# Kernel tuning notes

Hardware: AMD Instinct MI355X
Metric: run time of the kernel (lower is better)

## Reference

```python
import jax, jax.numpy as jnp
import numpy as np

NEG_SLOPE = 0.2
EPS = 1e-12


def _spmm(edge_row, edge_col, edge_w, h, n):
    # out[i] = sum_{e: row=i} w_e * h[col_e]   (row-normalized adjacency @ h)
    msgs = edge_w[:, None] * h[edge_col]
    return jax.ops.segment_sum(msgs, edge_row, num_segments=n)


def setup_inputs() -> dict:
    key = jax.random.key(0)
    ks = jax.random.split(key, 6)
    n, e, c_in, c_hid, c_out = 50000, 1600000, 300, 2048, 2048
    x = jax.random.normal(ks[0], (n, c_in), dtype=jnp.float32)
    # xavier-uniform-like init
    W1 = jax.random.uniform(ks[1], (c_in, c_hid), jnp.float32, -1.0, 1.0) * np.sqrt(6.0 / (c_in + c_hid))
    b1 = jnp.zeros((c_hid,), jnp.float32)
    W2 = jax.random.uniform(ks[2], (c_hid, c_out), jnp.float32, -1.0, 1.0) * np.sqrt(6.0 / (c_hid + c_out))
    b2 = jnp.zeros((c_out,), jnp.float32)
    edge_row = jax.random.randint(ks[3], (e,), 0, n, dtype=jnp.int32)
    edge_col = jax.random.randint(ks[4], (e,), 0, n, dtype=jnp.int32)
    return {"x": x, "W1": W1, "b1": b1, "W2": W2, "b2": b2,
            "edge_row": edge_row, "edge_col": edge_col}


def reference(x, W1, b1, W2, b2, edge_row, edge_col):
    n = x.shape[0]
    # 'in' normalization of unit-weight adjacency: w_e = 1 / in_degree(row_e)
    deg = jax.ops.segment_sum(jnp.ones_like(edge_row, dtype=jnp.float32), edge_row, num_segments=n)
    edge_w = 1.0 / jnp.maximum(deg, 1.0)
    edge_w = edge_w[edge_row]
    # layer 1: adj @ (x @ W1) + b1, LeakyReLU(0.2)  (dropout is identity in eval)
    h = _spmm(edge_row, edge_col, edge_w, x @ W1, n) + b1
    h = jnp.where(h >= 0, h, NEG_SLOPE * h)
    # last layer: no relu
    h = _spmm(edge_row, edge_col, edge_w, h @ W2, n) + b2
    # F.normalize: row-wise L2 with eps clamp
    norm = jnp.maximum(jnp.sqrt(jnp.sum(h * h, axis=-1, keepdims=True)), EPS)
    return h / norm
```

## Files before the change

### kernel.cpp

```cpp
#include <hip/hip_runtime.h>
#include <math.h>

typedef unsigned short ushort_t;
using bf16x8  = __attribute__((ext_vector_type(8))) short;
using f32x4   = __attribute__((ext_vector_type(4))) float;
using ushort8 = __attribute__((ext_vector_type(8))) unsigned short;

__device__ __forceinline__ unsigned short f2bf(float f) {
    union { float f; unsigned int u; } v; v.f = f;
    unsigned int r = v.u + 0x7FFFu + ((v.u >> 16) & 1u);
    return (unsigned short)(r >> 16);
}
__device__ __forceinline__ float bf2f(unsigned short u) {
    union { unsigned int u; float f; } v; v.u = ((unsigned int)u) << 16;
    return v.f;
}

#if defined(__has_builtin)
#if __has_builtin(__builtin_amdgcn_cvt_f32_fp8) && __has_builtin(__builtin_amdgcn_cvt_pk_fp8_f32)
#define FP8_HW 1
#endif
#endif

__device__ __forceinline__ unsigned char f2fp8(float v) {
#ifdef FP8_HW
    unsigned int p = __builtin_amdgcn_cvt_pk_fp8_f32(v, v, 0, false);
    return (unsigned char)(p & 0xFFu);
#else
    union { float f; unsigned u; } b; b.f = v;
    unsigned s = (b.u >> 24) & 0x80u;
    float a = fabsf(v);
    if (a >= 448.f) return (unsigned char)(s | 0x7E);
    if (a < 0.015625f) {
        int m = (int)rintf(a * 512.0f);
        if (m >= 8) return (unsigned char)(s | 0x08);
        return (unsigned char)(s | (unsigned)m);
    }
    unsigned u = b.u & 0x7FFFFFFFu;
    u += 0x7FFFFu + ((u >> 20) & 1u);
    int e8 = (int)((u >> 23) & 0xFF) - 120;
    unsigned M = (u >> 20) & 7u;
    if (e8 > 15 || (e8 == 15 && M == 7u)) return (unsigned char)(s | 0x7E);
    return (unsigned char)(s | ((unsigned)e8 << 3) | M);
#endif
}

#ifdef FP8_HW
#define ACC8(ac, w) do { \
    ac[0] += __builtin_amdgcn_cvt_f32_fp8((int)(w).x, 0); \
    ac[1] += __builtin_amdgcn_cvt_f32_fp8((int)(w).x, 1); \
    ac[2] += __builtin_amdgcn_cvt_f32_fp8((int)(w).x, 2); \
    ac[3] += __builtin_amdgcn_cvt_f32_fp8((int)(w).x, 3); \
    ac[4] += __builtin_amdgcn_cvt_f32_fp8((int)(w).y, 0); \
    ac[5] += __builtin_amdgcn_cvt_f32_fp8((int)(w).y, 1); \
    ac[6] += __builtin_amdgcn_cvt_f32_fp8((int)(w).y, 2); \
    ac[7] += __builtin_amdgcn_cvt_f32_fp8((int)(w).y, 3); \
} while (0)
#else
__device__ __forceinline__ float fp82f(unsigned u) {
    unsigned s = u >> 7, e = (u >> 3) & 15u, m = u & 7u;
    union { unsigned u; float f; } nb;
    nb.u = (s << 31) | ((e + 120u) << 23) | (m << 20);
    float sub = (float)(int)m * 0.001953125f;
    sub = s ? -sub : sub;
    return e ? nb.f : sub;
}
#define ACC8(ac, w) do { \
    ac[0] += fp82f(((w).x      ) & 0xFFu); \
    ac[1] += fp82f(((w).x >>  8) & 0xFFu); \
    ac[2] += fp82f(((w).x >> 16) & 0xFFu); \
    ac[3] += fp82f(((w).x >> 24)        ); \
    ac[4] += fp82f(((w).y      ) & 0xFFu); \
    ac[5] += fp82f(((w).y >>  8) & 0xFFu); \
    ac[6] += fp82f(((w).y >> 16) & 0xFFu); \
    ac[7] += fp82f(((w).y >> 24)        ); \
} while (0)
#endif

typedef const __attribute__((address_space(1))) void* gas_ptr;
typedef __attribute__((address_space(3))) void* las_ptr;
__device__ __forceinline__ void gload16(const void* g, void* l) {
    __builtin_amdgcn_global_load_lds((gas_ptr)g, (las_ptr)l, 16, 0, 0);
}


__global__ void k_zero_i32(int* __restrict__ p, int n) {
    int i = blockIdx.x * blockDim.x + threadIdx.x;
    if (i < n) p[i] = 0;
}

__global__ void k_count_deg(const int* __restrict__ erow, int* __restrict__ deg, int e) {
    for (int i = blockIdx.x * blockDim.x + threadIdx.x; i < e; i += gridDim.x * blockDim.x)
        atomicAdd(&deg[erow[i]], 1);
}

__global__ __launch_bounds__(1024) void k_scan(const int* __restrict__ deg, int* __restrict__ ptr,
                                               int* __restrict__ cursor, int n) {
    __shared__ int buf[1024];
    __shared__ int carry_s;
    int t = threadIdx.x;
    if (t == 0) { carry_s = 0; ptr[0] = 0; }
    __syncthreads();
    for (int base = 0; base < n; base += 1024) {
        int i = base + t;
        int v = (i < n) ? deg[i] : 0;
        buf[t] = v;
        __syncthreads();
        #pragma unroll
        for (int off = 1; off < 1024; off <<= 1) {
            int xv = (t >= off) ? buf[t - off] : 0;
            __syncthreads();
            buf[t] += xv;
            __syncthreads();
        }
        int carry = carry_s;
        int incl = buf[t] + carry;
        if (i < n) { ptr[i + 1] = incl; cursor[i] = incl - v; }
        int bsum = buf[1023];
        __syncthreads();
        if (t == 0) carry_s = carry + bsum;
        __syncthreads();
    }
}

__global__ void k_scatter(const int* __restrict__ erow, const int* __restrict__ ecol,
                          int* __restrict__ cursor, int* __restrict__ csr_col, int e) {
    for (int i = blockIdx.x * blockDim.x + threadIdx.x; i < e; i += gridDim.x * blockDim.x) {
        int pos = atomicAdd(&cursor[erow[i]], 1);
        csr_col[pos] = ecol[i];
    }
}


__global__ __launch_bounds__(256) void k_cvt_wT(const float* __restrict__ W, unsigned short* __restrict__ WT,
                                                int K, int N, int Kpad) {
    __shared__ float tile[32][33];
    int kp0 = blockIdx.x * 32, n0 = blockIdx.y * 32;
    int tx = threadIdx.x & 31, ty = threadIdx.x >> 5;
    #pragma unroll
    for (int ii = 0; ii < 4; ++ii) {
        int k = kp0 + ty + ii * 8;
        tile[ty + ii * 8][tx] = (k < K) ? W[(size_t)k * N + n0 + tx] : 0.0f;
    }
    __syncthreads();
    #pragma unroll
    for (int ii = 0; ii < 4; ++ii) {
        int n = n0 + ty + ii * 8;
        WT[(size_t)n * Kpad + kp0 + tx] = f2bf(tile[tx][ty + ii * 8]);
    }
}


__global__ __launch_bounds__(128) void k_spmm1(const int* __restrict__ ptr, const int* __restrict__ col,
                                               const float* __restrict__ x, unsigned short* __restrict__ ax) {
    int r = blockIdx.x;
    int t = threadIdx.x;
    int s = ptr[r], e = ptr[r + 1];
    bool act = t < 75;
    const float4* xb = (const float4*)x;
    float4 a0 = {0.f, 0.f, 0.f, 0.f}, a1 = {0.f, 0.f, 0.f, 0.f};
    int p = s;
    for (; p + 1 < e; p += 2) {
        int c0 = col[p], c1 = col[p + 1];
        if (act) {
            float4 v0 = xb[(size_t)c0 * 75 + t];
            float4 v1 = xb[(size_t)c1 * 75 + t];
            a0.x += v0.x; a0.y += v0.y; a0.z += v0.z; a0.w += v0.w;
            a1.x += v1.x; a1.y += v1.y; a1.z += v1.z; a1.w += v1.w;
        }
    }
    if (p < e && act) {
        float4 v = xb[(size_t)col[p] * 75 + t];
        a0.x += v.x; a0.y += v.y; a0.z += v.z; a0.w += v.w;
    }
    float w = 1.0f / fmaxf((float)(e - s), 1.0f);
    unsigned short* o = ax + (size_t)r * 320;
    if (act) {
        ushort4 ov;
        ov.x = f2bf((a0.x + a1.x) * w);
        ov.y = f2bf((a0.y + a1.y) * w);
        ov.z = f2bf((a0.z + a1.z) * w);
        ov.w = f2bf((a0.w + a1.w) * w);
        *(ushort4*)(o + t * 4) = ov;
    } else if (t < 80) {
        ushort4 z = {0, 0, 0, 0};
        *(ushort4*)(o + t * 4) = z;
    }
}


template <int EPI>
__global__ __launch_bounds__(256) void k_mfma_gemm(const unsigned short* __restrict__ A, int lda,
                                                   const unsigned short* __restrict__ BT, int ldb,
                                                   const float* __restrict__ bias,
                                                   void* __restrict__ Cv,
                                                   int M, int N, int K) {
    __shared__ __align__(16) unsigned short As[128 * 32];
    __shared__ __align__(16) unsigned short Bs[128 * 32];
    int tid = threadIdx.x;
    int lane = tid & 63;
    int wid = tid >> 6;
    int wm = wid >> 1, wn = wid & 1;
    int bm = blockIdx.y * 128, bn = blockIdx.x * 128;

    f32x4 zero4 = {0.f, 0.f, 0.f, 0.f};
    f32x4 acc[4][4];
    #pragma unroll
    for (int i = 0; i < 4; ++i)
        #pragma unroll
        for (int j = 0; j < 4; ++j) acc[i][j] = zero4;

    int srow = tid >> 2;
    int scol = (tid & 3) * 8;
    int ar0 = bm + srow;      if (ar0 >= M) ar0 = M - 1;
    int ar1 = bm + srow + 64; if (ar1 >= M) ar1 = M - 1;
    const unsigned short* gA0 = A + (size_t)ar0 * lda + scol;
    const unsigned short* gA1 = A + (size_t)ar1 * lda + scol;
    const unsigned short* gB0 = BT + (size_t)(bn + srow) * ldb + scol;
    const unsigned short* gB1 = BT + (size_t)(bn + srow + 64) * ldb + scol;

    int kq = (lane >> 4) * 8;
    int rsel = lane & 15;

    for (int k0 = 0; k0 < K; k0 += 32) {
        gload16(gA0 + k0, &As[(size_t)tid * 8]);
        gload16(gA1 + k0, &As[(size_t)(tid + 256) * 8]);
        gload16(gB0 + k0, &Bs[(size_t)tid * 8]);
        gload16(gB1 + k0, &Bs[(size_t)(tid + 256) * 8]);
        __syncthreads();

        bf16x8 af[4], bfr[4];
        #pragma unroll
        for (int i = 0; i < 4; ++i) {
            af[i]  = *(const bf16x8*)&As[(wm * 64 + i * 16 + rsel) * 32 + kq];
            bfr[i] = *(const bf16x8*)&Bs[(wn * 64 + i * 16 + rsel) * 32 + kq];
        }
        #pragma unroll
        for (int i = 0; i < 4; ++i)
            #pragma unroll
            for (int j = 0; j < 4; ++j)
                acc[i][j] = __builtin_amdgcn_mfma_f32_16x16x32_bf16(af[i], bfr[j], acc[i][j], 0, 0, 0);
        __syncthreads();
    }

    #pragma unroll
    for (int i = 0; i < 4; ++i) {
        int row_base = bm + wm * 64 + i * 16 + (lane >> 4) * 4;
        #pragma unroll
        for (int j = 0; j < 4; ++j) {
            int colg = bn + wn * 64 + j * 16 + (lane & 15);
            float bv = (EPI == 1) ? bias[colg] : 0.0f;
            #pragma unroll
            for (int r = 0; r < 4; ++r) {
                int row = row_base + r;
                if (row < M) {
                    float v = acc[i][j][r];
                    if (EPI == 1) {
                        v += bv; v = (v >= 0.f) ? v : 0.2f * v;
                        ((unsigned short*)Cv)[(size_t)row * N + colg] = f2bf(v);
                    } else {
                        ((unsigned char*)Cv)[(size_t)row * N + colg] = f2fp8(v * 32.0f);
                    }
                }
            }
        }
    }
}


__global__ __launch_bounds__(256) void k_spmm2_norm(const int* __restrict__ ptr, const int* __restrict__ col,
                                                    const unsigned char* __restrict__ H2,
                                                    const float* __restrict__ b2,
                                                    float* __restrict__ out) {
    const int C = 2048;
    int r = blockIdx.x, t = threadIdx.x;
    int s = ptr[r], e = ptr[r + 1];
    float ac0[8] = {}, ac1[8] = {}, ac2[8] = {}, ac3[8] = {};
    const uint2* base = (const uint2*)(H2 + t * 8);
    int p = s;
    for (; p + 3 < e; p += 4) {
        uint2 w0 = base[(size_t)col[p]     * 256];
        uint2 w1 = base[(size_t)col[p + 1] * 256];
        uint2 w2 = base[(size_t)col[p + 2] * 256];
        uint2 w3 = base[(size_t)col[p + 3] * 256];
        ACC8(ac0, w0); ACC8(ac1, w1); ACC8(ac2, w2); ACC8(ac3, w3);
    }
    for (; p < e; ++p) {
        uint2 w = base[(size_t)col[p] * 256];
        ACC8(ac0, w);
    }
    float w = 1.0f / (32.0f * fmaxf((float)(e - s), 1.0f));
    float ss = 0.f;
    float vv[8];
    #pragma unroll
    for (int j = 0; j < 8; ++j) {
        float v = (ac0[j] + ac1[j] + ac2[j] + ac3[j]) * w + b2[t * 8 + j];
        vv[j] = v;
        ss += v * v;
    }
    __shared__ float red[4];
    __shared__ float scale_s;
    #pragma unroll
    for (int off = 32; off > 0; off >>= 1) ss += __shfl_down(ss, off, 64);
    int lane = t & 63, wid = t >> 6;
    if (lane == 0) red[wid] = ss;
    __syncthreads();
    if (t == 0) {
        float tot = red[0] + red[1] + red[2] + red[3];
        scale_s = 1.0f / fmaxf(sqrtf(tot), 1e-12f);
    }
    __syncthreads();
    float sc = scale_s;
    float* o = out + (size_t)r * C + t * 8;
    float4 o0 = {vv[0] * sc, vv[1] * sc, vv[2] * sc, vv[3] * sc};
    float4 o1 = {vv[4] * sc, vv[5] * sc, vv[6] * sc, vv[7] * sc};
    *(float4*)o = o0;
    *(float4*)(o + 4) = o1;
}


extern "C" void kernel_launch(void* const* d_in, const int* in_sizes, int n_in,
                              void* d_out, int out_size, void* d_ws, size_t ws_size,
                              hipStream_t stream) {
    const float* x  = (const float*)d_in[0];
    const float* W1 = (const float*)d_in[1];
    const float* b1 = (const float*)d_in[2];
    const float* W2 = (const float*)d_in[3];
    const float* b2 = (const float*)d_in[4];
    const int* erow = (const int*)d_in[5];
    const int* ecol = (const int*)d_in[6];

    const int chid = in_sizes[2];
    const int cout = in_sizes[4];
    const int cin  = in_sizes[1] / chid;
    const int n    = in_sizes[0] / cin;
    const int e    = in_sizes[5];
    const int cinp = (cin + 31) & ~31;

    char* ws = (char*)d_ws;
    size_t off = 0;
    auto alloc = [&](size_t bytes) -> void* {
        void* p = ws + off;
        off += (bytes + 255) & ~(size_t)255;
        return p;
    };
    int*            deg     = (int*)alloc((size_t)n * 4);
    int*            ptr     = (int*)alloc((size_t)(n + 1) * 4);
    int*            cursor  = (int*)alloc((size_t)n * 4);
    int*            csr_col = (int*)alloc((size_t)e * 4);
    unsigned short* ax      = (unsigned short*)alloc((size_t)n * cinp * 2);
    unsigned short* W1T     = (unsigned short*)alloc((size_t)chid * cinp * 2);
    unsigned short* W2T     = (unsigned short*)alloc((size_t)cout * chid * 2);
    unsigned char*  H2f8    = (unsigned char*)alloc((size_t)n * cout);
    unsigned short* H1      = (unsigned short*)d_out;

    k_zero_i32<<<(n + 255) / 256, 256, 0, stream>>>(deg, n);
    k_count_deg<<<2048, 256, 0, stream>>>(erow, deg, e);
    k_scan<<<1, 1024, 0, stream>>>(deg, ptr, cursor, n);
    k_scatter<<<2048, 256, 0, stream>>>(erow, ecol, cursor, csr_col, e);

    dim3 gw1(cinp / 32, chid / 32);
    k_cvt_wT<<<gw1, 256, 0, stream>>>(W1, W1T, cin, chid, cinp);
    dim3 gw2(chid / 32, cout / 32);
    k_cvt_wT<<<gw2, 256, 0, stream>>>(W2, W2T, chid, cout, chid);

    k_spmm1<<<n, 128, 0, stream>>>(ptr, csr_col, x, ax);

    dim3 g1(chid / 128, (n + 127) / 128);
    k_mfma_gemm<1><<<g1, 256, 0, stream>>>(ax, cinp, W1T, cinp, b1, (void*)H1, n, chid, cinp);

    dim3 g2(cout / 128, (n + 127) / 128);
    k_mfma_gemm<2><<<g2, 256, 0, stream>>>(H1, chid, W2T, chid, (const float*)nullptr, (void*)H2f8, n, cout, chid);

    k_spmm2_norm<<<n, 256, 0, stream>>>(ptr, csr_col, H2f8, b2, (float*)d_out);
}
```

Measured before the change: 1.823 ms.

## Use 256x256-tile 8-wave bf16 MFMA GEMM with double-buffered LDS for layer 2

Replaces the 128x128 tile GEMM for the second layer (n x 2048 x 2048) with a new 512-thread kernel computing 256x256 output tiles. It uses 8 waves, each owning a 128x64 sub-tile, and K split into two 32-wide phases. Global-to-LDS loads go through a swizzled, double-buffered layout and are prefetched during compute, with MFMA issue given raised priority. The goal is more reuse per loaded byte and better overlap of loads with matrix math in the dominant GEMM. The cost is a large register footprint (128 accumulator floats per thread) and 128KB of LDS, which limits occupancy.

```diff
diff --git a/kernel.cpp b/kernel.cpp
--- a/kernel.cpp
+++ b/kernel.cpp
@@ -268,6 +268,106 @@
 }
 
 
+__global__ __launch_bounds__(512) void k_gemm8p_fp8(const unsigned short* __restrict__ A, int lda,
+                                                    const unsigned short* __restrict__ BT, int ldb,
+                                                    unsigned char* __restrict__ C,
+                                                    int M, int N, int K) {
+    __shared__ __align__(16) unsigned short As_l[2][2][8192];
+    __shared__ __align__(16) unsigned short Bs_l[2][2][8192];
+
+    const int tid  = threadIdx.x;
+    const int lane = tid & 63;
+    const int wid  = tid >> 6;
+    const int wm   = wid >> 2;
+    const int wn   = wid & 3;
+    const int bm = blockIdx.y * 256, bn = blockIdx.x * 256;
+
+    int rA[2], rB[2], cc[2], ldst[2];
+    #pragma unroll
+    for (int i = 0; i < 2; ++i) {
+        int P = wid * 2048 + i * 1024 + lane * 16;
+        int L = P ^ (((P >> 7) & 3) << 4);
+        int r = L >> 6;
+        cc[i] = (L & 63) >> 1;
+        int ra = bm + r; if (ra >= M) ra = M - 1;
+        rA[i] = ra;
+        rB[i] = bn + r;
+        ldst[i] = P >> 1;
+    }
+
+    const int rsel = lane & 15, kq8 = (lane >> 4) * 8;
+    int aoff[8], boff[4];
+    #pragma unroll
+    for (int fi = 0; fi < 8; ++fi) {
+        int row = wm * 128 + fi * 16 + rsel;
+        aoff[fi] = row * 32 + (kq8 ^ (((row >> 1) & 3) << 3));
+    }
+    #pragma unroll
+    for (int fj = 0; fj < 4; ++fj) {
+        int row = wn * 64 + fj * 16 + rsel;
+        boff[fj] = row * 32 + (kq8 ^ (((row >> 1) & 3) << 3));
+    }
+
+    f32x4 acc[8][4];
+    #pragma unroll
+    for (int fi = 0; fi < 8; ++fi)
+        #pragma unroll
+        for (int fj = 0; fj < 4; ++fj) { f32x4 z = {0.f,0.f,0.f,0.f}; acc[fi][fj] = z; }
+
+    #define STAGE_K(buf, h, k0) do { \
+        gload16(A  + (size_t)rA[0] * lda + (k0) + (h) * 32 + cc[0], &As_l[buf][h][ldst[0]]); \
+        gload16(A  + (size_t)rA[1] * lda + (k0) + (h) * 32 + cc[1], &As_l[buf][h][ldst[1]]); \
+        gload16(BT + (size_t)rB[0] * ldb + (k0) + (h) * 32 + cc[0], &Bs_l[buf][h][ldst[0]]); \
+        gload16(BT + (size_t)rB[1] * ldb + (k0) + (h) * 32 + cc[1], &Bs_l[buf][h][ldst[1]]); \
+    } while (0)
+
+    const int NT = K / 64;
+
+    STAGE_K(0, 0, 0);
+    STAGE_K(0, 1, 0);
+    asm volatile("s_waitcnt vmcnt(4)\n\ts_barrier" ::: "memory");
+
+    for (int t = 0; t < NT; ++t) {
+        const int bt = t & 1;
+        const int kn = (t + 1) * 64;
+        const bool pf = (t + 1 < NT);
+        #pragma unroll
+        for (int ph = 0; ph < 2; ++ph) {
+            if (pf) STAGE_K(bt ^ 1, ph, kn);
+            bf16x8 af[8], bfv[4];
+            #pragma unroll
+            for (int fi = 0; fi < 8; ++fi) af[fi] = *(const bf16x8*)&As_l[bt][ph][aoff[fi]];
+            #pragma unroll
+            for (int fj = 0; fj < 4; ++fj) bfv[fj] = *(const bf16x8*)&Bs_l[bt][ph][boff[fj]];
+            __builtin_amdgcn_s_setprio(1);
+            #pragma unroll
+            for (int fi = 0; fi < 8; ++fi)
+                #pragma unroll
+                for (int fj = 0; fj < 4; ++fj)
+                    acc[fi][fj] = __builtin_amdgcn_mfma_f32_16x16x32_bf16(af[fi], bfv[fj], acc[fi][fj], 0, 0, 0);
+            __builtin_amdgcn_s_setprio(0);
+            if (pf)                 asm volatile("s_waitcnt vmcnt(4)\n\ts_barrier" ::: "memory");
+            else if (ph == 0)       asm volatile("s_waitcnt vmcnt(0)\n\ts_barrier" ::: "memory");
+        }
+    }
+    #undef STAGE_K
+
+    #pragma unroll
+    for (int fi = 0; fi < 8; ++fi) {
+        int row_base = bm + wm * 128 + fi * 16 + (lane >> 4) * 4;
+        #pragma unroll
+        for (int fj = 0; fj < 4; ++fj) {
+            int colg = bn + wn * 64 + fj * 16 + (lane & 15);
+            #pragma unroll
+            for (int r = 0; r < 4; ++r) {
+                int row = row_base + r;
+                if (row < M) C[(size_t)row * N + colg] = f2fp8(acc[fi][fj][r] * 32.0f);
+            }
+        }
+    }
+}
+
+
 __global__ __launch_bounds__(256) void k_spmm2_norm(const int* __restrict__ ptr, const int* __restrict__ col,
                                                     const unsigned char* __restrict__ H2,
                                                     const float* __restrict__ b2,
@@ -369,8 +469,8 @@
     dim3 g1(chid / 128, (n + 127) / 128);
     k_mfma_gemm<1><<<g1, 256, 0, stream>>>(ax, cinp, W1T, cinp, b1, (void*)H1, n, chid, cinp);
 
-    dim3 g2(cout / 128, (n + 127) / 128);
-    k_mfma_gemm<2><<<g2, 256, 0, stream>>>(H1, chid, W2T, chid, (const float*)nullptr, (void*)H2f8, n, cout, chid);
+    dim3 g2(cout / 256, (n + 255) / 256);
+    k_gemm8p_fp8<<<g2, 512, 0, stream>>>(H1, chid, W2T, chid, H2f8, n, cout, chid);
 
     k_spmm2_norm<<<n, 256, 0, stream>>>(ptr, csr_col, H2f8, b2, (float*)d_out);
 }
```

After: 1.855 ms. About the same (+1.7%).
